# Kernel optimization log

Hardware: AMD Instinct MI355X
Metric: run time of the kernel (lower is better)

Reference implementation:

```python
import jax, jax.numpy as jnp
import numpy as np

LAM = 0.5
EPS = 1e-6


def setup_inputs() -> dict:
    key = jax.random.key(0)
    k1, k2 = jax.random.split(key)
    shape = (32, 1, 480, 640)
    prediction = jax.random.uniform(k1, shape, dtype=jnp.float32)
    target = jax.random.uniform(k2, shape, dtype=jnp.float32)
    return {"prediction": prediction, "target": target}


def reference(prediction, target):
    B = prediction.shape[0]
    p = prediction.reshape(B, -1)
    t = target.reshape(B, -1)
    mask = t > 0  # valid pixels
    # safe masked log-diff (avoid NaN from log of masked-out entries)
    ld = jnp.where(mask,
                   jnp.log(jnp.where(mask, p, 1.0) + EPS)
                   - jnp.log(jnp.where(mask, t, 1.0) + EPS),
                   0.0)
    cnt = jnp.sum(mask, axis=1).astype(p.dtype)          # [B]
    safe_cnt = jnp.maximum(cnt, 1.0)
    mean_sq = jnp.sum(ld * ld, axis=1) / safe_cnt        # mean(log_diff^2)
    mean_ld = jnp.sum(ld, axis=1) / safe_cnt             # mean(log_diff)
    per_sample = mean_sq - LAM * mean_ld * mean_ld
    per_sample = jnp.where(cnt > 0, per_sample, 0.0)     # skip empty masks
    return jnp.sum(per_sample) / B
```

## Files before the change

### kernel.cpp

```cpp
#include <hip/hip_runtime.h>

#define NSAMP 32
#define NELEM 307200
#define LAM 0.5f
#define EPS 1e-6f
#define BLOCKS_PER_SAMPLE 32
#define THREADS 256


__global__ __launch_bounds__(THREADS)
void sill_partial(const float* __restrict__ pred,
                  const float* __restrict__ targ,
                  float4* __restrict__ ws) {
    const int b     = blockIdx.y;
    const int chunk = blockIdx.x;
    const int tid   = threadIdx.x;

    const int f4_per_sample = NELEM / 4;
    const int f4_per_block  = f4_per_sample / BLOCKS_PER_SAMPLE;

    const float4* p4 = (const float4*)(pred + (size_t)b * NELEM) + (size_t)chunk * f4_per_block;
    const float4* t4 = (const float4*)(targ + (size_t)b * NELEM) + (size_t)chunk * f4_per_block;

    float s1 = 0.f, s2 = 0.f, c = 0.f;

    for (int i = tid; i < f4_per_block; i += THREADS) {
        float4 p = p4[i];
        float4 t = t4[i];
        if (t.x > 0.f) { float ld = __logf(p.x + EPS) - __logf(t.x + EPS); s1 += ld; s2 += ld * ld; c += 1.f; }
        if (t.y > 0.f) { float ld = __logf(p.y + EPS) - __logf(t.y + EPS); s1 += ld; s2 += ld * ld; c += 1.f; }
        if (t.z > 0.f) { float ld = __logf(p.z + EPS) - __logf(t.z + EPS); s1 += ld; s2 += ld * ld; c += 1.f; }
        if (t.w > 0.f) { float ld = __logf(p.w + EPS) - __logf(t.w + EPS); s1 += ld; s2 += ld * ld; c += 1.f; }
    }

    #pragma unroll
    for (int off = 32; off > 0; off >>= 1) {
        s1 += __shfl_down(s1, off);
        s2 += __shfl_down(s2, off);
        c  += __shfl_down(c,  off);
    }

    __shared__ float sh1[THREADS / 64];
    __shared__ float sh2[THREADS / 64];
    __shared__ float shc[THREADS / 64];
    const int wave = tid >> 6;
    if ((tid & 63) == 0) { sh1[wave] = s1; sh2[wave] = s2; shc[wave] = c; }
    __syncthreads();

    if (tid == 0) {
        float a1 = 0.f, a2 = 0.f, ac = 0.f;
        #pragma unroll
        for (int w = 0; w < THREADS / 64; ++w) { a1 += sh1[w]; a2 += sh2[w]; ac += shc[w]; }
        ws[b * BLOCKS_PER_SAMPLE + chunk] = make_float4(a1, a2, ac, 0.f);
    }
}

__global__ __launch_bounds__(1024)
void sill_final(const float4* __restrict__ ws, float* __restrict__ out) {
    const int t = threadIdx.x;
    float4 part = ws[t];

    #pragma unroll
    for (int off = 16; off > 0; off >>= 1) {
        part.x += __shfl_down(part.x, off, 32);
        part.y += __shfl_down(part.y, off, 32);
        part.z += __shfl_down(part.z, off, 32);
    }

    __shared__ float ps_sh[NSAMP];
    if ((t & 31) == 0) {
        float cnt = part.z;
        float sc  = fmaxf(cnt, 1.f);
        float ml  = part.x / sc;
        float ms  = part.y / sc;
        float ps  = ms - LAM * ml * ml;
        ps_sh[t >> 5] = (cnt > 0.f) ? ps : 0.f;
    }
    __syncthreads();

    if (t < 64) {
        float v = (t < NSAMP) ? ps_sh[t] : 0.f;
        #pragma unroll
        for (int off = 32; off > 0; off >>= 1) v += __shfl_down(v, off);
        if (t == 0) out[0] = v / (float)NSAMP;
    }
}

extern "C" void kernel_launch(void* const* d_in, const int* in_sizes, int n_in,
                              void* d_out, int out_size, void* d_ws, size_t ws_size,
                              hipStream_t stream) {
    const float* pred = (const float*)d_in[0];
    const float* targ = (const float*)d_in[1];
    float* out  = (float*)d_out;
    float4* ws  = (float4*)d_ws;

    dim3 grid(BLOCKS_PER_SAMPLE, NSAMP);
    sill_partial<<<grid, THREADS, 0, stream>>>(pred, targ, ws);
    sill_final<<<1, 1024, 0, stream>>>(ws, out);
}
```

Before: 106.3 us.

## Flatten grid into many small blocks with upfront loads and branchless accumulation

Replaces the strided per-block loop with fixed-size blocks where each thread issues four float4 loads of each input before computing, giving many more blocks and more memory requests in flight. The masked log-diff is computed branchlessly via selects. The final reduction now sums a larger set of partials using shared-memory atomics. It trades extra partial results and atomic work in the final kernel for better memory-level parallelism in the main pass.

```diff
diff --git a/kernel.cpp b/kernel.cpp
--- a/kernel.cpp
+++ b/kernel.cpp
@@ -4,34 +4,52 @@
 #define NELEM 307200
 #define LAM 0.5f
 #define EPS 1e-6f
-#define BLOCKS_PER_SAMPLE 32
 #define THREADS 256
+#define F4_PER_THREAD 4
+#define F4_PER_BLOCK (THREADS * F4_PER_THREAD)
+#define BLOCKS_PER_SAMPLE ((NELEM / 4) / F4_PER_BLOCK)
+#define NBLOCKS (NSAMP * BLOCKS_PER_SAMPLE)
 
 
-__global__ __launch_bounds__(THREADS)
+__device__ __forceinline__ void accum(float p, float t, float& s1, float& s2, float& c) {
+    bool m = t > 0.f;
+    float ld = __logf(p + EPS) - __logf(t + EPS);
+    ld = m ? ld : 0.f;
+    s1 += ld;
+    s2 += ld * ld;
+    c  += m ? 1.f : 0.f;
+}
+
+__global__ __launch_bounds__(THREADS, 8)
 void sill_partial(const float* __restrict__ pred,
                   const float* __restrict__ targ,
                   float4* __restrict__ ws) {
-    const int b     = blockIdx.y;
-    const int chunk = blockIdx.x;
-    const int tid   = threadIdx.x;
+    const int blk = blockIdx.x;
+    const int b   = blk / BLOCKS_PER_SAMPLE;
+    const int j   = blk % BLOCKS_PER_SAMPLE;
+    const int tid = threadIdx.x;
 
-    const int f4_per_sample = NELEM / 4;
-    const int f4_per_block  = f4_per_sample / BLOCKS_PER_SAMPLE;
+    const float4* p4 = (const float4*)(pred + (size_t)b * NELEM) + (size_t)j * F4_PER_BLOCK;
+    const float4* t4 = (const float4*)(targ + (size_t)b * NELEM) + (size_t)j * F4_PER_BLOCK;
 
-    const float4* p4 = (const float4*)(pred + (size_t)b * NELEM) + (size_t)chunk * f4_per_block;
-    const float4* t4 = (const float4*)(targ + (size_t)b * NELEM) + (size_t)chunk * f4_per_block;
+    float4 p0 = p4[tid];
+    float4 p1 = p4[tid + THREADS];
+    float4 p2 = p4[tid + 2 * THREADS];
+    float4 p3 = p4[tid + 3 * THREADS];
+    float4 q0 = t4[tid];
+    float4 q1 = t4[tid + THREADS];
+    float4 q2 = t4[tid + 2 * THREADS];
+    float4 q3 = t4[tid + 3 * THREADS];
 
     float s1 = 0.f, s2 = 0.f, c = 0.f;
-
-    for (int i = tid; i < f4_per_block; i += THREADS) {
-        float4 p = p4[i];
-        float4 t = t4[i];
-        if (t.x > 0.f) { float ld = __logf(p.x + EPS) - __logf(t.x + EPS); s1 += ld; s2 += ld * ld; c += 1.f; }
-        if (t.y > 0.f) { float ld = __logf(p.y + EPS) - __logf(t.y + EPS); s1 += ld; s2 += ld * ld; c += 1.f; }
-        if (t.z > 0.f) { float ld = __logf(p.z + EPS) - __logf(t.z + EPS); s1 += ld; s2 += ld * ld; c += 1.f; }
-        if (t.w > 0.f) { float ld = __logf(p.w + EPS) - __logf(t.w + EPS); s1 += ld; s2 += ld * ld; c += 1.f; }
-    }
+    accum(p0.x, q0.x, s1, s2, c); accum(p0.y, q0.y, s1, s2, c);
+    accum(p0.z, q0.z, s1, s2, c); accum(p0.w, q0.w, s1, s2, c);
+    accum(p1.x, q1.x, s1, s2, c); accum(p1.y, q1.y, s1, s2, c);
+    accum(p1.z, q1.z, s1, s2, c); accum(p1.w, q1.w, s1, s2, c);
+    accum(p2.x, q2.x, s1, s2, c); accum(p2.y, q2.y, s1, s2, c);
+    accum(p2.z, q2.z, s1, s2, c); accum(p2.w, q2.w, s1, s2, c);
+    accum(p3.x, q3.x, s1, s2, c); accum(p3.y, q3.y, s1, s2, c);
+    accum(p3.z, q3.z, s1, s2, c); accum(p3.w, q3.w, s1, s2, c);
 
     #pragma unroll
     for (int off = 32; off > 0; off >>= 1) {
@@ -51,37 +69,38 @@
         float a1 = 0.f, a2 = 0.f, ac = 0.f;
         #pragma unroll
         for (int w = 0; w < THREADS / 64; ++w) { a1 += sh1[w]; a2 += sh2[w]; ac += shc[w]; }
-        ws[b * BLOCKS_PER_SAMPLE + chunk] = make_float4(a1, a2, ac, 0.f);
+        ws[blk] = make_float4(a1, a2, ac, 0.f);
     }
 }
 
 __global__ __launch_bounds__(1024)
 void sill_final(const float4* __restrict__ ws, float* __restrict__ out) {
     const int t = threadIdx.x;
-    float4 part = ws[t];
+    __shared__ float acc[NSAMP * 4];
 
-    #pragma unroll
-    for (int off = 16; off > 0; off >>= 1) {
-        part.x += __shfl_down(part.x, off, 32);
-        part.y += __shfl_down(part.y, off, 32);
-        part.z += __shfl_down(part.z, off, 32);
-    }
+    if (t < NSAMP * 4) acc[t] = 0.f;
+    __syncthreads();
 
-    __shared__ float ps_sh[NSAMP];
-    if ((t & 31) == 0) {
-        float cnt = part.z;
-        float sc  = fmaxf(cnt, 1.f);
-        float ml  = part.x / sc;
-        float ms  = part.y / sc;
-        float ps  = ms - LAM * ml * ml;
-        ps_sh[t >> 5] = (cnt > 0.f) ? ps : 0.f;
+    for (int idx = t; idx < NBLOCKS; idx += 1024) {
+        float4 part = ws[idx];
+        int s = idx / BLOCKS_PER_SAMPLE;
+        atomicAdd(&acc[s * 4 + 0], part.x);
+        atomicAdd(&acc[s * 4 + 1], part.y);
+        atomicAdd(&acc[s * 4 + 2], part.z);
     }
     __syncthreads();
 
-    if (t < 64) {
-        float v = (t < NSAMP) ? ps_sh[t] : 0.f;
+    if (t < NSAMP) {
+        float s1  = acc[t * 4 + 0];
+        float s2  = acc[t * 4 + 1];
+        float cnt = acc[t * 4 + 2];
+        float sc  = fmaxf(cnt, 1.f);
+        float ml  = s1 / sc;
+        float ms  = s2 / sc;
+        float ps  = ms - LAM * ml * ml;
+        float v   = (cnt > 0.f) ? ps : 0.f;
         #pragma unroll
-        for (int off = 32; off > 0; off >>= 1) v += __shfl_down(v, off);
+        for (int off = 16; off > 0; off >>= 1) v += __shfl_down(v, off, 32);
         if (t == 0) out[0] = v / (float)NSAMP;
     }
 }
@@ -91,10 +110,9 @@
                               hipStream_t stream) {
     const float* pred = (const float*)d_in[0];
     const float* targ = (const float*)d_in[1];
-    float* out  = (float*)d_out;
-    float4* ws  = (float4*)d_ws;
+    float* out = (float*)d_out;
+    float4* ws = (float4*)d_ws;
 
-    dim3 grid(BLOCKS_PER_SAMPLE, NSAMP);
-    sill_partial<<<grid, THREADS, 0, stream>>>(pred, targ, ws);
+    sill_partial<<<NBLOCKS, THREADS, 0, stream>>>(pred, targ, ws);
     sill_final<<<1, 1024, 0, stream>>>(ws, out);
 }
```

Measured after the change: 109.2 us. 2.7% more time.
